# Kernel tuning notes

Measured on AMD Instinct MI355X. Metric: run time of the kernel, lower is better.

The kernel has to match this reference:

```python
import jax, jax.numpy as jnp
import numpy as np

B, T = 4096, 35          # batch rallies, max_ball_round
DSE = 227                # state_embed_dim = (37-2) + 64 + 64 + 64
C = 64                   # context_dim
H = 1024                 # hidden_dim
G5 = 25                  # GMM_num * 5
S = 12                   # shot_num
SE_NOCTX = DSE - C       # 163, state_embedding features before prior_z concat


def setup_inputs() -> dict:
    key = jax.random.key(0)
    ks = jax.random.split(key, 24)
    def r(i, shape, s=0.05):
        return (jax.random.normal(ks[i], shape, jnp.float32) * s)
    return {
        "state_embedding": r(0, (B, T, SE_NOCTX), 1.0),
        "prior_z": r(1, (B, C), 1.0),
        # state_ref_encoder (no bias)
        "W_ref": r(2, (T * DSE, DSE), 0.01),
        # f_decoder: DSE -> H -> H -> DSE with Softplus
        "fW1": r(3, (DSE, H)), "fb1": jnp.zeros((H,), jnp.float32),
        "fW2": r(4, (H, H)),   "fb2": jnp.zeros((H,), jnp.float32),
        "fW3": r(5, (H, DSE)), "fb3": jnp.zeros((DSE,), jnp.float32),
        # g_nets: DSE independent Linear(1,DSE)->Softplus->Linear(DSE,1)->Sigmoid, stacked
        "gW1": r(6, (DSE, DSE), 0.01), "gb1": r(7, (DSE, DSE), 0.01),
        "gW2": r(8, (DSE, DSE), 0.01), "gb2": r(9, (DSE,), 0.01),
        # GMM / shot heads on f_latent (no bias)
        "W_land": r(10, (DSE, G5), 0.01),
        "W_shot": r(11, (DSE, S), 0.01),
        "W_move": r(12, (DSE, G5), 0.01),
        # context_decoder: C -> H -> H -> C with Softplus
        "cW1": r(13, (C, H)), "cb1": jnp.zeros((H,), jnp.float32),
        "cW2": r(14, (H, H)), "cb2": jnp.zeros((H,), jnp.float32),
        "cW3": r(15, (H, C)), "cb3": jnp.zeros((C,), jnp.float32),
        # context GMM / shot heads (no bias)
        "cW_land": r(16, (C, G5), 0.01),
        "cW_shot": r(17, (C, S), 0.01),
        "cW_move": r(18, (C, G5), 0.01),
    }


def reference(state_embedding, prior_z, W_ref,
              fW1, fb1, fW2, fb2, fW3, fb3,
              gW1, gb1, gW2, gb2,
              W_land, W_shot, W_move,
              cW1, cb1, cW2, cb2, cW3, cb3,
              cW_land, cW_shot, cW_move):
    sp = jax.nn.softplus
    b, t, _ = state_embedding.shape

    # context_decoder(prior_z)
    ch = sp(prior_z @ cW1 + cb1)
    ch = sp(ch @ cW2 + cb2)
    ctx = ch @ cW3 + cb3                                  # [B, C]

    # repeat prior_z along time, concat, flatten, state_ref_encoder
    prior_rep = jnp.broadcast_to(prior_z[:, None, :], (b, t, prior_z.shape[-1]))
    sre = jnp.concatenate([state_embedding, prior_rep], axis=-1)  # [B, T, DSE]
    f_input = sre.reshape(b, -1) @ W_ref                  # [B, DSE]

    # f_decoder
    fh = sp(f_input @ fW1 + fb1)
    fh = sp(fh @ fW2 + fb2)
    f_latent = fh @ fW3 + fb3                             # [B, DSE]

    # g(): DSE per-dim tiny MLPs, fully vectorized as batched einsum
    gh = sp(f_latent[:, :, None] * gW1[None, :, :] + gb1[None, :, :])  # [B, DSE, DSE]
    g_out = jax.nn.sigmoid(jnp.einsum('bdh,dh->bd', gh, gW2) + gb2)    # [B, DSE]

    # GMM / shot heads
    land = f_latent @ W_land                              # [B, 25]
    shot = jax.nn.log_softmax(f_latent @ W_shot, axis=-1) # [B, 12]
    move = f_latent @ W_move                              # [B, 25]
    c_land = ctx @ cW_land
    c_shot = jax.nn.log_softmax(ctx @ cW_shot, axis=-1)
    c_move = ctx @ cW_move

    return jnp.concatenate([land, shot, move, g_out, c_land, c_shot, c_move, ctx], axis=-1)  # [B, 415]
```

## Files before the change

kernel.cpp:

```cpp
#include <hip/hip_runtime.h>
#include <hip/hip_bf16.h>

using s8 = __attribute__((ext_vector_type(8))) short;
using f4 = __attribute__((ext_vector_type(4))) float;
using us8 = __attribute__((ext_vector_type(8))) unsigned short;

__device__ __forceinline__ void glds16(const void* g, void* l) {
    __builtin_amdgcn_global_load_lds(
        (const __attribute__((address_space(1))) void*)g,
        (__attribute__((address_space(3))) void*)l, 16, 0, 0);
}

__device__ __forceinline__ unsigned short f2b(float f) {
    union { float f; unsigned u; } v; v.f = f;
    unsigned r = v.u + 0x7fffu + ((v.u >> 16) & 1u);
    return (unsigned short)(r >> 16);
}
__device__ __forceinline__ float softplus_f(float x) {
    return fmaxf(x, 0.f) + __logf(1.f + __expf(-fabsf(x)));
}
__device__ __forceinline__ float sigmoid_f(float x) {
    return 1.f / (1.f + __expf(-x));
}
__device__ __forceinline__ float exp2_f(float x) {
    float r; asm("v_exp_f32 %0, %1" : "=v"(r) : "v"(x)); return r;
}
__device__ __forceinline__ float log2_f(float x) {
    float r; asm("v_log_f32 %0, %1" : "=v"(r) : "v"(x)); return r;
}

__global__ __launch_bounds__(256) void transpose_w(const float* __restrict__ src,
                                                   unsigned short* __restrict__ dst,
                                                   int K, int N, int Kpad, int Npad) {
    __shared__ float tile[32][33];
    const int n0 = blockIdx.x * 32, k0 = blockIdx.y * 32;
    const int tx = threadIdx.x, ty = threadIdx.y;
#pragma unroll
    for (int r = 0; r < 4; r++) {
        int k = k0 + ty + r * 8, n = n0 + tx;
        tile[ty + r * 8][tx] = (k < K && n < N) ? src[(size_t)k * N + n] : 0.f;
    }
    __syncthreads();
#pragma unroll
    for (int r = 0; r < 4; r++) {
        int n = n0 + ty + r * 8, k = k0 + tx;
        if (n < Npad && k < Kpad) dst[(size_t)n * Kpad + k] = f2b(tile[tx][ty + r * 8]);
    }
}

__global__ __launch_bounds__(256) void prep6_k(
    const float* __restrict__ s0, const float* __restrict__ s1,
    const float* __restrict__ s2, const float* __restrict__ s3,
    const float* __restrict__ s4, const float* __restrict__ s5,
    unsigned short* __restrict__ d0, unsigned short* __restrict__ d1,
    unsigned short* __restrict__ d2, unsigned short* __restrict__ d3,
    unsigned short* __restrict__ d4, unsigned short* __restrict__ d5) {
    constexpr int Ks[6] = {64, 1024, 1024, 227, 1024, 1024};
    constexpr int Ns[6] = {1024, 1024, 64, 1024, 1024, 227};
    constexpr int Kp[6] = {64, 1024, 1024, 256, 1024, 1024};
    constexpr int Np[6] = {1024, 1024, 128, 1024, 1024, 256};
    const int z = blockIdx.z;
    const int K = Ks[z], N = Ns[z], Kpad = Kp[z], Npad = Np[z];
    if ((int)blockIdx.x >= Npad / 32 || (int)blockIdx.y >= Kpad / 32) return;
    const float* src = z == 0 ? s0 : z == 1 ? s1 : z == 2 ? s2 : z == 3 ? s3 : z == 4 ? s4 : s5;
    unsigned short* dst = z == 0 ? d0 : z == 1 ? d1 : z == 2 ? d2 : z == 3 ? d3 : z == 4 ? d4 : d5;
    __shared__ float tile[32][33];
    const int n0 = blockIdx.x * 32, k0 = blockIdx.y * 32;
    const int tx = threadIdx.x, ty = threadIdx.y;
#pragma unroll
    for (int r = 0; r < 4; r++) {
        int k = k0 + ty + r * 8, n = n0 + tx;
        tile[ty + r * 8][tx] = (k < K && n < N) ? src[(size_t)k * N + n] : 0.f;
    }
    __syncthreads();
#pragma unroll
    for (int r = 0; r < 4; r++) {
        int n = n0 + ty + r * 8, k = k0 + tx;
        dst[(size_t)n * Kpad + k] = f2b(tile[tx][ty + r * 8]);
    }
}

__global__ __launch_bounds__(256) void wcat_t(const float* __restrict__ Wref,
                                              unsigned short* __restrict__ dst) {
    __shared__ float tile[32][33];
    const int n0 = blockIdx.x * 32, k0 = blockIdx.y * 32;
    const int tx = threadIdx.x, ty = threadIdx.y;
#pragma unroll
    for (int r = 0; r < 4; r++) {
        int k = k0 + ty + r * 8, n = n0 + tx;
        float v = 0.f;
        if (n < 227 && k < 5769) {
            if (k < 5705) {
                int wrow = k + 64 * (k / 163);
                v = Wref[(size_t)wrow * 227 + n];
            } else {
                int j2 = k - 5705;
                for (int t = 0; t < 35; t++)
                    v += Wref[(size_t)(t * 227 + 163 + j2) * 227 + n];
            }
        }
        tile[ty + r * 8][tx] = v;
    }
    __syncthreads();
#pragma unroll
    for (int r = 0; r < 4; r++) {
        int n = n0 + ty + r * 8, k = k0 + tx;
        if (n < 256 && k < 5792) dst[(size_t)n * 5792 + k] = f2b(tile[tx][ty + r * 8]);
    }
}

__global__ __launch_bounds__(256) void misc_k(
    const float* __restrict__ pz, unsigned short* __restrict__ pzb,
    const float* __restrict__ gb1, const float* __restrict__ gW2,
    float* __restrict__ b1s, float* __restrict__ w2s,
    const float* __restrict__ Wl, const float* __restrict__ Ws, const float* __restrict__ Wm,
    const float* __restrict__ cWl, const float* __restrict__ cWs, const float* __restrict__ cWm,
    unsigned short* __restrict__ WhcT) {
    constexpr int NCVT = 4096 * 64;
    constexpr int NGS = 227 * 227;
    constexpr int NW = 128 * 320;
    int i = blockIdx.x * 256 + threadIdx.x;
    if (i < NCVT) {
        pzb[i] = f2b(pz[i]);
    } else if (i < NCVT + NGS) {
        int j = i - NCVT;
        b1s[j] = gb1[j] * 1.44269504f;
        w2s[j] = gW2[j] * 0.69314718f;
    } else if (i < NCVT + NGS + NW) {
        int j = i - NCVT - NGS;
        int n = j / 320, k = j - n * 320;
        float v = 0.f;
        if (n < 62 && k < 227) {
            if (n < 25)      v = Wl[(size_t)k * 25 + n];
            else if (n < 37) v = Ws[(size_t)k * 12 + (n - 25)];
            else             v = Wm[(size_t)k * 25 + (n - 37)];
        } else if (n >= 64 && n < 126 && k >= 256) {
            const int jj = n - 64, kk = k - 256;
            if (jj < 25)      v = cWl[(size_t)kk * 25 + jj];
            else if (jj < 37) v = cWs[(size_t)kk * 12 + (jj - 25)];
            else              v = cWm[(size_t)kk * 25 + (jj - 37)];
        }
        WhcT[(size_t)n * 320 + k] = f2b(v);
    }
}

__global__ __launch_bounds__(256) void acat_k8(const float* __restrict__ se,
                                               const float* __restrict__ pz,
                                               unsigned short* __restrict__ dst) {
    const int row = blockIdx.y;
    const int c = blockIdx.x * 256 + threadIdx.x;
    if (c >= 724) return;
    const int col0 = c * 8;
    us8 o;
    if (col0 + 8 <= 5705) {
        const float* s = se + (size_t)row * 5705 + col0;
#pragma unroll
        for (int j = 0; j < 8; j++) o[j] = f2b(s[j]);
    } else {
#pragma unroll
        for (int j = 0; j < 8; j++) {
            int col = col0 + j;
            float v = 0.f;
            if (col < 5705) v = se[(size_t)row * 5705 + col];
            else if (col < 5769) v = pz[(size_t)row * 64 + (col - 5705)];
            o[j] = f2b(v);
        }
    }
    *(us8*)(dst + (size_t)row * 5792 + col0) = o;
}

__global__ __launch_bounds__(256) void finb_k(const float* __restrict__ fin,
                                              unsigned short* __restrict__ out) {
    const int row = blockIdx.y, col = threadIdx.x;
    out[(size_t)row * 256 + col] = (col < 227) ? f2b(fin[(size_t)row * 228 + col])
                                               : (unsigned short)0;
}

__global__ __launch_bounds__(256) void fillb_k(float* __restrict__ buf,
                                               const float* __restrict__ bias,
                                               int ld, int ncr) {
    const int row = blockIdx.y;
    const int col = blockIdx.x * 256 + threadIdx.x;
    if (col >= ld) return;
    float v = 0.f;
    if (bias && col < ncr) v = bias[col];
    buf[(size_t)row * ld + col] = v;
}

__global__ __launch_bounds__(256) void gscale_k(const float* __restrict__ gb1,
                                                const float* __restrict__ gW2,
                                                float* __restrict__ b1s,
                                                float* __restrict__ w2s) {
    int i = blockIdx.x * 256 + threadIdx.x;
    if (i < 227 * 227) {
        b1s[i] = gb1[i] * 1.44269504f;
        w2s[i] = gW2[i] * 0.69314718f;
    }
}

__global__ __launch_bounds__(256) void red_enc4(const float* __restrict__ part,
                                                unsigned short* __restrict__ finb) {
    const int t = threadIdx.x;
    const int row = blockIdx.y * 4 + (t >> 6);
    const int cw = t & 63;
    if (cw < 57) {
        const float* p = part + (size_t)row * 228 + cw * 4;
        float4 s = make_float4(0.f, 0.f, 0.f, 0.f);
#pragma unroll
        for (int z = 0; z < 6; z++) {
            float4 v = *(const float4*)(p + (size_t)z * 4096 * 228);
            s.x += v.x; s.y += v.y; s.z += v.z; s.w += v.w;
        }
        if (cw == 56) s.w = 0.f;
        ushort4 o;
        o.x = f2b(s.x); o.y = f2b(s.y); o.z = f2b(s.z); o.w = f2b(s.w);
        *(ushort4*)(finb + (size_t)row * 256 + cw * 4) = o;
    } else {
        ushort4 z4 = make_ushort4(0, 0, 0, 0);
        *(ushort4*)(finb + (size_t)row * 256 + 228 + (cw - 57) * 4) = z4;
    }
}

__global__ __launch_bounds__(256) void red_cf3_k(
    const float* __restrict__ part_c3, const float* __restrict__ cb3,
    float* __restrict__ ctxb,
    const float* __restrict__ part_f3, const float* __restrict__ fb3,
    float* __restrict__ flat) {
    const int bx = blockIdx.x, t = threadIdx.x;
    if (bx < 256) {
        int idx = bx * 256 + t;
        int row = idx >> 4, c4 = idx & 15;
        float4 s = *(const float4*)(cb3 + c4 * 4);
        const float* p = part_c3 + (size_t)row * 64 + c4 * 4;
#pragma unroll
        for (int z = 0; z < 8; z++) {
            float4 v = *(const float4*)(p + (size_t)z * 4096 * 64);
            s.x += v.x; s.y += v.y; s.z += v.z; s.w += v.w;
        }
        *(float4*)(ctxb + (size_t)row * 64 + c4 * 4) = s;
    } else {
        const int by = bx - 256;
        const int row = by * 4 + (t >> 6);
        const int cw = t & 63;
        if (cw >= 57) return;
        float b[4];
#pragma unroll
        for (int j = 0; j < 4; j++) {
            int col = cw * 4 + j;
            b[j] = (col < 227) ? fb3[col] : 0.f;
        }
        const float* p = part_f3 + (size_t)row * 228 + cw * 4;
        float4 s = make_float4(b[0], b[1], b[2], b[3]);
#pragma unroll
        for (int z = 0; z < 4; z++) {
            float4 v = *(const float4*)(p + (size_t)z * 4096 * 228);
            s.x += v.x; s.y += v.y; s.z += v.z; s.w += v.w;
        }
        if (cw == 56) s.w = 0.f;
        *(float4*)(flat + (size_t)row * 228 + cw * 4) = s;
    }
}

__global__ __launch_bounds__(320) void ah_k(const float* __restrict__ flat,
                                            const float* __restrict__ ctx,
                                            unsigned short* __restrict__ dst) {
    const int b = blockIdx.x, t = threadIdx.x;
    float v = 0.f;
    if (t < 227) v = flat[(size_t)b * 228 + t];
    else if (t >= 256) v = ctx[(size_t)b * 64 + (t - 256)];
    dst[(size_t)b * 320 + t] = f2b(v);
}

__device__ __forceinline__ float lse12(const float* s) {
    float m = s[0];
#pragma unroll
    for (int j = 1; j < 12; j++) m = fmaxf(m, s[j]);
    float sum = 0.f;
#pragma unroll
    for (int j = 0; j < 12; j++) sum += __expf(s[j] - m);
    return m + __logf(sum);
}

__global__ __launch_bounds__(192) void final_k(const float* __restrict__ raw,
                                               const float* __restrict__ ctx,
                                               float* __restrict__ out) {
    __shared__ float s[12], c[12];
    const int b = blockIdx.x, t = threadIdx.x;
    float* ob = out + (size_t)b * 415;
    const float* rb = raw + (size_t)b * 128;
    if (t < 62) {
        float v = rb[t];
        if (t < 25) ob[t] = v;
        else if (t < 37) s[t - 25] = v;
        else ob[t] = v;
    } else if (t >= 64 && t < 126) {
        const int j2 = t - 64;
        float v = rb[t];
        if (j2 < 25) ob[289 + j2] = v;
        else if (j2 < 37) c[j2 - 25] = v;
        else ob[289 + j2] = v;
    } else if (t >= 128) {
        ob[351 + (t - 128)] = ctx[(size_t)b * 64 + (t - 128)];
    }
    __syncthreads();
    if (t < 12) {
        ob[25 + t] = s[t] - lse12(s);
    } else if (t >= 64 && t < 76) {
        ob[314 + (t - 64)] = c[t - 64] - lse12(c);
    }
}

template <int CM, int ACT, bool OBF16>
__global__ __launch_bounds__(256) void gemm_dma(
    const unsigned short* __restrict__ A, int lda,
    const unsigned short* __restrict__ WT, int ldwt,
    const float* __restrict__ bias,
    void* __restrict__ Cptr, int ldc, int N, int K, int kchunk) {
    __shared__ __align__(16) unsigned short As[128 * 32];
    __shared__ __align__(16) unsigned short Bs[128 * 32];
    const int tid = threadIdx.x;
    const int m0 = blockIdx.y * 128, n0 = blockIdx.x * 128;
    const int kbeg = blockIdx.z * kchunk;
    const int kend = min(kbeg + kchunk, K);
    const int lane = tid & 63, w = tid >> 6;
    const int wm = w >> 1, wn = w & 1;
    const int quad = lane >> 4, l16 = lane & 15;
    const int dr = lane >> 2;
    const int dk = (lane & 3) * 8;

    f4 acc[4][4] = {};

    for (int k0 = kbeg; k0 < kend; k0 += 32) {
#pragma unroll
        for (int c = 0; c < 2; c++) {
            int rr = w * 32 + c * 16;
            glds16(A + (size_t)(m0 + rr + dr) * lda + k0 + dk, &As[rr * 32]);
            glds16(WT + (size_t)(n0 + rr + dr) * ldwt + k0 + dk, &Bs[rr * 32]);
        }
        __syncthreads();
        s8 a[4], b[4];
#pragma unroll
        for (int mi = 0; mi < 4; mi++)
            a[mi] = *(const s8*)&As[(wm * 64 + mi * 16 + l16) * 32 + quad * 8];
#pragma unroll
        for (int ni = 0; ni < 4; ni++)
            b[ni] = *(const s8*)&Bs[(wn * 64 + ni * 16 + l16) * 32 + quad * 8];
#pragma unroll
        for (int mi = 0; mi < 4; mi++)
#pragma unroll
            for (int ni = 0; ni < 4; ni++)
                acc[mi][ni] = __builtin_amdgcn_mfma_f32_16x16x32_bf16(
                    a[mi], b[ni], acc[mi][ni], 0, 0, 0);
        __syncthreads();
    }

    const size_t zoff = (CM == 2) ? (size_t)blockIdx.z * 4096 * ldc : 0;
#pragma unroll
    for (int mi = 0; mi < 4; mi++) {
        int gmb = m0 + wm * 64 + mi * 16 + quad * 4;
#pragma unroll
        for (int ni = 0; ni < 4; ni++) {
            int gn = n0 + wn * 64 + ni * 16 + l16;
            if (gn < N) {
#pragma unroll
                for (int r = 0; r < 4; r++) {
                    float v = acc[mi][ni][r];
                    size_t off = (size_t)(gmb + r) * ldc + gn;
                    if (CM == 2) {
                        ((float*)Cptr)[zoff + off] = v;
                    } else {
                        if (bias) v += bias[gn];
                        if (ACT == 1) v = softplus_f(v);
                        if (OBF16) ((unsigned short*)Cptr)[off] = f2b(v);
                        else ((float*)Cptr)[off] = v;
                    }
                }
            }
        }
    }
}

__global__ __launch_bounds__(256) void gemm_dualg(
    const unsigned short* __restrict__ A0, int lda0, int K0,
    const unsigned short* __restrict__ A1, int lda1, int K1,
    const unsigned short* __restrict__ W0, int ldw0,
    const unsigned short* __restrict__ W1, int ldw1,
    const float* __restrict__ b0, const float* __restrict__ b1,
    unsigned short* __restrict__ C0, unsigned short* __restrict__ C1) {
    __shared__ __align__(16) unsigned short As[128 * 32];
    __shared__ __align__(16) unsigned short Bs[128 * 32];
    const int z = blockIdx.z;
// ... 37 lines not shown
                    a[mi], b[ni], acc[mi][ni], 0, 0, 0);
        __syncthreads();
    }

#pragma unroll
    for (int mi = 0; mi < 4; mi++) {
        int gmb = m0 + wm * 64 + mi * 16 + quad * 4;
#pragma unroll
        for (int ni = 0; ni < 4; ni++) {
            int gn = n0 + wn * 64 + ni * 16 + l16;
#pragma unroll
            for (int r = 0; r < 4; r++) {
                float v = acc[mi][ni][r] + bias[gn];
                C[(size_t)(gmb + r) * 1024 + gn] = f2b(softplus_f(v));
            }
        }
    }
}

__global__ __launch_bounds__(256) void part_cf3_k(
    const unsigned short* __restrict__ h2c, const unsigned short* __restrict__ cW3T,
    const unsigned short* __restrict__ h2f, const unsigned short* __restrict__ fW3T,
    float* __restrict__ part_c3, float* __restrict__ part_f3) {
    __shared__ __align__(16) unsigned short As[128 * 32];
    __shared__ __align__(16) unsigned short Bs[128 * 32];
    const int z = blockIdx.z;
    const bool isC = (z < 8);
    if (isC && blockIdx.x != 0) return;
    const unsigned short* __restrict__ A  = isC ? h2c : h2f;
    const unsigned short* __restrict__ WT = isC ? cW3T : fW3T;
    const int N   = isC ? 64 : 227;
    const int ldc = isC ? 64 : 228;
    const int zz  = isC ? z : z - 8;
    const int kbeg = zz * (isC ? 128 : 256);
    const int kend = kbeg + (isC ? 128 : 256);
    float* __restrict__ C = (isC ? part_c3 : part_f3) + (size_t)zz * 4096 * ldc;
    const int tid = threadIdx.x;
    const int m0 = blockIdx.y * 128, n0 = blockIdx.x * 128;
    const int lane = tid & 63, w = tid >> 6;
    const int wm = w >> 1, wn = w & 1;
    const int quad = lane >> 4, l16 = lane & 15;
    const int dr = lane >> 2;
    const int dk = (lane & 3) * 8;

    f4 acc[4][4] = {};

    for (int k0 = kbeg; k0 < kend; k0 += 32) {
#pragma unroll
        for (int c = 0; c < 2; c++) {
            int rr = w * 32 + c * 16;
            glds16(A + (size_t)(m0 + rr + dr) * 1024 + k0 + dk, &As[rr * 32]);
            glds16(WT + (size_t)(n0 + rr + dr) * 1024 + k0 + dk, &Bs[rr * 32]);
        }
        __syncthreads();
        s8 a[4], b[4];
#pragma unroll
        for (int mi = 0; mi < 4; mi++)
            a[mi] = *(const s8*)&As[(wm * 64 + mi * 16 + l16) * 32 + quad * 8];
#pragma unroll
        for (int ni = 0; ni < 4; ni++)
            b[ni] = *(const s8*)&Bs[(wn * 64 + ni * 16 + l16) * 32 + quad * 8];
#pragma unroll
        for (int mi = 0; mi < 4; mi++)
#pragma unroll
            for (int ni = 0; ni < 4; ni++)
                acc[mi][ni] = __builtin_amdgcn_mfma_f32_16x16x32_bf16(
                    a[mi], b[ni], acc[mi][ni], 0, 0, 0);
        __syncthreads();
    }

#pragma unroll
    for (int mi = 0; mi < 4; mi++) {
        int gmb = m0 + wm * 64 + mi * 16 + quad * 4;
#pragma unroll
        for (int ni = 0; ni < 4; ni++) {
            int gn = n0 + wn * 64 + ni * 16 + l16;
            if (gn < N) {
#pragma unroll
                for (int r = 0; r < 4; r++)
                    C[(size_t)(gmb + r) * ldc + gn] = acc[mi][ni][r];
            }
        }
    }
}

template <int AMODE, int ACT, bool ATOMIC, bool OBF16>
__global__ __launch_bounds__(256) void gemm_mfma(
    const void* __restrict__ Aptr, int lda,
    const float* __restrict__ A2ptr,
    const unsigned short* __restrict__ WT, int ldwt,
    const float* __restrict__ bias,
    void* __restrict__ Cptr, int ldc,
    int M, int N, int K, int kchunk) {
    __shared__ unsigned short As[128 * 40];
    __shared__ unsigned short Bs[128 * 40];
    const int tid = threadIdx.x;
    const int m0 = blockIdx.y * 128, n0 = blockIdx.x * 128;
    const int kbeg = blockIdx.z * kchunk;
    const int kend = min(kbeg + kchunk, K);
    const int lane = tid & 63, w = tid >> 6;
    const int wm = w >> 1, wn = w & 1;
    const int quad = lane >> 4, l16 = lane & 15;

    f4 acc[4][4] = {};
    ushort4 pa[4], pb[4];

    auto loadA = [&](int k0) {
        const bool full = (kend - k0) >= 32;
#pragma unroll
        for (int i = 0; i < 4; i++) {
            int f = tid + i * 256;
            int r = f >> 3, cc = (f & 7) * 4;
            int gm = m0 + r;
            ushort4 val;
            if (AMODE == 0) {
                const float* A = (const float*)Aptr;
                float t[4];
#pragma unroll
                for (int j = 0; j < 4; j++) {
                    int k = k0 + cc + j;
                    t[j] = (k < kend) ? A[(size_t)gm * lda + k] : 0.f;
                }
                val.x = f2b(t[0]); val.y = f2b(t[1]); val.z = f2b(t[2]); val.w = f2b(t[3]);
            } else if (AMODE == 1) {
                const unsigned short* A = (const unsigned short*)Aptr;
                if (full) {
                    val = *(const ushort4*)(A + (size_t)gm * lda + k0 + cc);
                } else {
                    unsigned short t[4];
#pragma unroll
                    for (int j = 0; j < 4; j++) {
                        int k = k0 + cc + j;
                        t[j] = (k < kend) ? A[(size_t)gm * lda + k] : (unsigned short)0;
                    }
                    val.x = t[0]; val.y = t[1]; val.z = t[2]; val.w = t[3];
                }
            } else {
                const float* se = (const float*)Aptr;
                float t[4];
#pragma unroll
                for (int j = 0; j < 4; j++) {
                    int k = k0 + cc + j;
                    float v = 0.f;
                    if (k < kend) {
                        v = (k < 5705) ? se[(size_t)gm * 5705 + k]
                                       : A2ptr[(size_t)gm * 64 + (k - 5705)];
                    }
                    t[j] = v;
                }
                val.x = f2b(t[0]); val.y = f2b(t[1]); val.z = f2b(t[2]); val.w = f2b(t[3]);
            }
            pa[i] = val;
        }
    };
    auto loadB = [&](int k0) {
        const bool full = (kend - k0) >= 32;
#pragma unroll
        for (int i = 0; i < 4; i++) {
            int f = tid + i * 256;
            int r = f >> 3, cc = (f & 7) * 4;
            int gn = n0 + r;
            ushort4 val;
            if (gn < N) {
                if (full) {
                    val = *(const ushort4*)(WT + (size_t)gn * ldwt + k0 + cc);
                } else {
// ... 139 lines not shown
            for (int k = 0; k < 64; k++) a = fmaf(cx[k], cWl[(size_t)k * 25 + j2], a);
            ob[289 + j2] = a;
        } else if (j2 < 37) {
            int j = j2 - 25;
            float a = 0.f;
            for (int k = 0; k < 64; k++) a = fmaf(cx[k], cWsh[(size_t)k * 12 + j], a);
            craw[j] = a;
        } else {
            int j = j2 - 37;
            float a = 0.f;
            for (int k = 0; k < 64; k++) a = fmaf(cx[k], cWm[(size_t)k * 25 + j], a);
            ob[326 + j] = a;
        }
    } else if (t >= 128 && t < 192) {
        ob[351 + (t - 128)] = cx[t - 128];
    }
    __syncthreads();
    if (t == 0) lsf = lse12(sraw);
    if (t == 64) lsc = lse12(craw);
    __syncthreads();
    if (t < 12) ob[25 + t] = sraw[t] - lsf;
    else if (t >= 64 && t < 76) ob[314 + (t - 64)] = craw[t - 64] - lsc;
}

extern "C" void kernel_launch(void* const* d_in, const int* in_sizes, int n_in,
                              void* d_out, int out_size, void* d_ws, size_t ws_size,
                              hipStream_t stream) {
    const float* se    = (const float*)d_in[0];
    const float* pz    = (const float*)d_in[1];
    const float* Wref  = (const float*)d_in[2];
    const float* fW1   = (const float*)d_in[3];
    const float* fb1   = (const float*)d_in[4];
    const float* fW2   = (const float*)d_in[5];
    const float* fb2   = (const float*)d_in[6];
    const float* fW3   = (const float*)d_in[7];
    const float* fb3   = (const float*)d_in[8];
    const float* gW1   = (const float*)d_in[9];
    const float* gb1   = (const float*)d_in[10];
    const float* gW2   = (const float*)d_in[11];
    const float* gb2   = (const float*)d_in[12];
    const float* Wland = (const float*)d_in[13];
    const float* Wshot = (const float*)d_in[14];
    const float* Wmove = (const float*)d_in[15];
    const float* cW1   = (const float*)d_in[16];
    const float* cb1   = (const float*)d_in[17];
    const float* cW2   = (const float*)d_in[18];
    const float* cb2   = (const float*)d_in[19];
    const float* cW3   = (const float*)d_in[20];
    const float* cb3   = (const float*)d_in[21];
    const float* cWl   = (const float*)d_in[22];
    const float* cWs   = (const float*)d_in[23];
    const float* cWm   = (const float*)d_in[24];
    float* out = (float*)d_out;
    const int M = 4096;

    char* p = (char*)d_ws;
    auto alloc = [&](size_t bytes) {
        char* r = p;
        p += (bytes + 255) & ~(size_t)255;
        return r;
    };
    unsigned short* WcatT = (unsigned short*)alloc((size_t)256 * 5792 * 2);
    unsigned short* cW1T  = (unsigned short*)alloc((size_t)1024 * 64 * 2);
    unsigned short* cW2T  = (unsigned short*)alloc((size_t)1024 * 1024 * 2);
    unsigned short* cW3T  = (unsigned short*)alloc((size_t)128 * 1024 * 2);
    unsigned short* fW1T  = (unsigned short*)alloc((size_t)1024 * 256 * 2);
    unsigned short* fW2T  = (unsigned short*)alloc((size_t)1024 * 1024 * 2);
    unsigned short* fW3T  = (unsigned short*)alloc((size_t)256 * 1024 * 2);
    float* fin  = (float*)alloc((size_t)M * 228 * 4);
    float* flat = (float*)alloc((size_t)M * 228 * 4);
    float* ctxb = (float*)alloc((size_t)M * 64 * 4);
    unsigned short* h2b  = (unsigned short*)alloc((size_t)M * 1024 * 2);
    unsigned short* h1fb = (unsigned short*)alloc((size_t)M * 1024 * 2);
    float* b1s = (float*)alloc((size_t)227 * 227 * 4);
    float* w2s = (float*)alloc((size_t)227 * 227 * 4);

    size_t base_used = (size_t)(p - (char*)d_ws);
    size_t full_extra = (size_t)M * 64 * 2
                      + (size_t)M * 256 * 2
                      + (size_t)M * 5792 * 2
                      + (size_t)128 * 320 * 2 + 1024;
    const bool full = (base_used + full_extra + 65536) <= ws_size;

    prep6_k<<<dim3(32, 32, 6), dim3(32, 8), 0, stream>>>(
        cW1, cW2, cW3, fW1, fW2, fW3, cW1T, cW2T, cW3T, fW1T, fW2T, fW3T);
    wcat_t<<<dim3(8, 181), dim3(32, 8), 0, stream>>>(Wref, WcatT);

    if (full) {
        unsigned short* pzb  = (unsigned short*)alloc((size_t)M * 64 * 2);
        unsigned short* finb = (unsigned short*)alloc((size_t)M * 256 * 2);
        char* region = alloc((size_t)M * 5792 * 2);
        unsigned short* WhcT = (unsigned short*)alloc((size_t)128 * 320 * 2);
        unsigned short* Acat = (unsigned short*)region;
        float* part_enc = fin;
        unsigned short* h2fb   = (unsigned short*)region;
        float* part_c3         = (float*)(region + (size_t)8 * 1024 * 1024);
        unsigned short* h1f    = (unsigned short*)(region + (size_t)16 * 1024 * 1024);
        float* part_f3         = (float*)(region + (size_t)24 * 1024 * 1024);
        float* rawfc           = (float*)(region + (size_t)39 * 1024 * 1024);
        unsigned short* Ah     = (unsigned short*)(region + (size_t)41 * 1024 * 1024);
        unsigned short* h1c = h1fb;
        unsigned short* h2c = h2b;

        misc_k<<<dim3(1386), 256, 0, stream>>>(
            pz, pzb, gb1, gW2, b1s, w2s, Wland, Wshot, Wmove, cWl, cWs, cWm, WhcT);
        acat_k8<<<dim3(3, M), 256, 0, stream>>>(se, pz, Acat);

        gemm_dma<2, 0, false><<<dim3(2, 32, 6), 256, 0, stream>>>(
            Acat, 5792, WcatT, 5792, nullptr, part_enc, 228, 227, 5792, 992);
        red_enc4<<<dim3(1, 1024), 256, 0, stream>>>(part_enc, finb);

        gemm_dualg<<<dim3(8, 32, 2), 256, 0, stream>>>(
            pzb, 64, 64, finb, 256, 256, cW1T, 64, fW1T, 256, cb1, fb1, h1c, h1f);
        gemm_dualg<<<dim3(8, 32, 2), 256, 0, stream>>>(
            h1c, 1024, 1024, h1f, 1024, 1024, cW2T, 1024, fW2T, 1024, cb2, fb2, h2c, h2fb);

        part_cf3_k<<<dim3(2, 32, 12), 256, 0, stream>>>(
            h2c, cW3T, h2fb, fW3T, part_c3, part_f3);
        red_cf3_k<<<dim3(1280), 256, 0, stream>>>(
            part_c3, cb3, ctxb, part_f3, fb3, flat);

        g_kernel2<<<dim3(227, 8), 256, 0, stream>>>(flat, gW1, b1s, w2s, gb2, out);

        ah_k<<<dim3(4096), 320, 0, stream>>>(flat, ctxb, Ah);
        gemm_dma<0, 0, false><<<dim3(1, 32, 1), 256, 0, stream>>>(
            Ah, 320, WhcT, 320, nullptr, rawfc, 128, 126, 320, 320);
        final_k<<<dim3(4096), 192, 0, stream>>>(rawfc, ctxb, out);
    } else {
        gscale_k<<<dim3(202), 256, 0, stream>>>(gb1, gW2, b1s, w2s);
        fillb_k<<<dim3(1, M), 256, 0, stream>>>(fin, nullptr, 228, 0);
        fillb_k<<<dim3(1, M), 256, 0, stream>>>(flat, fb3, 228, 227);
        fillb_k<<<dim3(1, M), 256, 0, stream>>>(ctxb, cb3, 64, 64);
        unsigned short* h1 = h1fb;
        gemm_mfma<0, 1, false, true><<<dim3(8, 32, 1), 256, 0, stream>>>(
            pz, 64, nullptr, cW1T, 64, cb1, h1, 1024, M, 1024, 64, 64);
        gemm_mfma<1, 1, false, true><<<dim3(8, 32, 1), 256, 0, stream>>>(
            h1, 1024, nullptr, cW2T, 1024, cb2, h2b, 1024, M, 1024, 1024, 1024);
        gemm_mfma<1, 0, true, false><<<dim3(1, 32, 8), 256, 0, stream>>>(
            h2b, 1024, nullptr, cW3T, 1024, nullptr, ctxb, 64, M, 64, 1024, 128);
        gemm_mfma<2, 0, true, false><<<dim3(2, 32, 8), 256, 0, stream>>>(
            se, 5705, pz, WcatT, 5792, nullptr, fin, 228, M, 227, 5769, 736);
        gemm_mfma<0, 1, false, true><<<dim3(8, 32, 1), 256, 0, stream>>>(
            fin, 228, nullptr, fW1T, 256, fb1, h1, 1024, M, 1024, 227, 227);
        gemm_mfma<1, 1, false, true><<<dim3(8, 32, 1), 256, 0, stream>>>(
            h1, 1024, nullptr, fW2T, 1024, fb2, h2b, 1024, M, 1024, 1024, 1024);
        gemm_mfma<1, 0, true, false><<<dim3(2, 32, 8), 256, 0, stream>>>(
            h2b, 1024, nullptr, fW3T, 1024, nullptr, flat, 228, M, 227, 1024, 128);
        heads_k<<<dim3(4096), 256, 0, stream>>>(flat, ctxb, Wland, Wshot, Wmove,
                                                cWl, cWs, cWm, out);
        g_kernel2<<<dim3(227, 8), 256, 0, stream>>>(flat, gW1, b1s, w2s, gb2, out);
    }
}
```

Before: 410.0 us.

## Merge prep kernels into one launch and fuse tail stages into fewer kernels

Combines the weight transposes, Wref concat-transpose, misc conversions and activation bf16 packing into a single prep_all_k launch partitioned by block index. It also fuses the g-net evaluation with building the head input, and fuses the heads GEMM with the log-softmax and output scatter, removing the rawfc round trip and the final_k launch. The aim is to cut launch overhead and intermediate global traffic, at the cost of more branching inside the merged kernels and blocks of uneven cost sharing one grid.

```diff
diff --git a/kernel.cpp b/kernel.cpp
--- a/kernel.cpp
+++ b/kernel.cpp
@@ -29,172 +29,142 @@
     float r; asm("v_log_f32 %0, %1" : "=v"(r) : "v"(x)); return r;
 }
 
-__global__ __launch_bounds__(256) void transpose_w(const float* __restrict__ src,
-                                                   unsigned short* __restrict__ dst,
-                                                   int K, int N, int Kpad, int Npad) {
-    __shared__ float tile[32][33];
-    const int n0 = blockIdx.x * 32, k0 = blockIdx.y * 32;
-    const int tx = threadIdx.x, ty = threadIdx.y;
-#pragma unroll
-    for (int r = 0; r < 4; r++) {
-        int k = k0 + ty + r * 8, n = n0 + tx;
-        tile[ty + r * 8][tx] = (k < K && n < N) ? src[(size_t)k * N + n] : 0.f;
-    }
-    __syncthreads();
-#pragma unroll
-    for (int r = 0; r < 4; r++) {
-        int n = n0 + ty + r * 8, k = k0 + tx;
-        if (n < Npad && k < Kpad) dst[(size_t)n * Kpad + k] = f2b(tile[tx][ty + r * 8]);
-    }
-}
-
-__global__ __launch_bounds__(256) void prep6_k(
-    const float* __restrict__ s0, const float* __restrict__ s1,
-    const float* __restrict__ s2, const float* __restrict__ s3,
-    const float* __restrict__ s4, const float* __restrict__ s5,
-    unsigned short* __restrict__ d0, unsigned short* __restrict__ d1,
-    unsigned short* __restrict__ d2, unsigned short* __restrict__ d3,
-    unsigned short* __restrict__ d4, unsigned short* __restrict__ d5) {
-    constexpr int Ks[6] = {64, 1024, 1024, 227, 1024, 1024};
-    constexpr int Ns[6] = {1024, 1024, 64, 1024, 1024, 227};
-    constexpr int Kp[6] = {64, 1024, 1024, 256, 1024, 1024};
-    constexpr int Np[6] = {1024, 1024, 128, 1024, 1024, 256};
-    const int z = blockIdx.z;
-    const int K = Ks[z], N = Ns[z], Kpad = Kp[z], Npad = Np[z];
-    if ((int)blockIdx.x >= Npad / 32 || (int)blockIdx.y >= Kpad / 32) return;
-    const float* src = z == 0 ? s0 : z == 1 ? s1 : z == 2 ? s2 : z == 3 ? s3 : z == 4 ? s4 : s5;
-    unsigned short* dst = z == 0 ? d0 : z == 1 ? d1 : z == 2 ? d2 : z == 3 ? d3 : z == 4 ? d4 : d5;
-    __shared__ float tile[32][33];
-    const int n0 = blockIdx.x * 32, k0 = blockIdx.y * 32;
-    const int tx = threadIdx.x, ty = threadIdx.y;
-#pragma unroll
-    for (int r = 0; r < 4; r++) {
-        int k = k0 + ty + r * 8, n = n0 + tx;
-        tile[ty + r * 8][tx] = (k < K && n < N) ? src[(size_t)k * N + n] : 0.f;
-    }
-    __syncthreads();
-#pragma unroll
-    for (int r = 0; r < 4; r++) {
-        int n = n0 + ty + r * 8, k = k0 + tx;
-        dst[(size_t)n * Kpad + k] = f2b(tile[tx][ty + r * 8]);
-    }
-}
-
-__global__ __launch_bounds__(256) void wcat_t(const float* __restrict__ Wref,
-                                              unsigned short* __restrict__ dst) {
-    __shared__ float tile[32][33];
-    const int n0 = blockIdx.x * 32, k0 = blockIdx.y * 32;
-    const int tx = threadIdx.x, ty = threadIdx.y;
-#pragma unroll
-    for (int r = 0; r < 4; r++) {
-        int k = k0 + ty + r * 8, n = n0 + tx;
-        float v = 0.f;
-        if (n < 227 && k < 5769) {
-            if (k < 5705) {
-                int wrow = k + 64 * (k / 163);
-                v = Wref[(size_t)wrow * 227 + n];
-            } else {
-                int j2 = k - 5705;
-                for (int t = 0; t < 35; t++)
-                    v += Wref[(size_t)(t * 227 + 163 + j2) * 227 + n];
-            }
-        }
-        tile[ty + r * 8][tx] = v;
-    }
-    __syncthreads();
-#pragma unroll
-    for (int r = 0; r < 4; r++) {
-        int n = n0 + ty + r * 8, k = k0 + tx;
-        if (n < 256 && k < 5792) dst[(size_t)n * 5792 + k] = f2b(tile[tx][ty + r * 8]);
-    }
-}
-
-__global__ __launch_bounds__(256) void misc_k(
+__device__ __forceinline__ float lse12(const float* s) {
+    float m = s[0];
+#pragma unroll
+    for (int j = 1; j < 12; j++) m = fmaxf(m, s[j]);
+    float sum = 0.f;
+#pragma unroll
+    for (int j = 0; j < 12; j++) sum += __expf(s[j] - m);
+    return m + __logf(sum);
+}
+
+__global__ __launch_bounds__(256) void prep_all_k(
+    const float* __restrict__ cW1, const float* __restrict__ cW2,
+    const float* __restrict__ cW3, const float* __restrict__ fW1,
+    const float* __restrict__ fW2, const float* __restrict__ fW3,
+    unsigned short* __restrict__ cW1T, unsigned short* __restrict__ cW2T,
+    unsigned short* __restrict__ cW3T, unsigned short* __restrict__ fW1T,
+    unsigned short* __restrict__ fW2T, unsigned short* __restrict__ fW3T,
+    const float* __restrict__ Wref, unsigned short* __restrict__ WcatT,
     const float* __restrict__ pz, unsigned short* __restrict__ pzb,
     const float* __restrict__ gb1, const float* __restrict__ gW2,
     float* __restrict__ b1s, float* __restrict__ w2s,
-    const float* __restrict__ Wl, const float* __restrict__ Ws, const float* __restrict__ Wm,
-    const float* __restrict__ cWl, const float* __restrict__ cWs, const float* __restrict__ cWm,
-    unsigned short* __restrict__ WhcT) {
-    constexpr int NCVT = 4096 * 64;
-    constexpr int NGS = 227 * 227;
-    constexpr int NW = 128 * 320;
-    int i = blockIdx.x * 256 + threadIdx.x;
-    if (i < NCVT) {
-        pzb[i] = f2b(pz[i]);
-    } else if (i < NCVT + NGS) {
-        int j = i - NCVT;
-        b1s[j] = gb1[j] * 1.44269504f;
-        w2s[j] = gW2[j] * 0.69314718f;
-    } else if (i < NCVT + NGS + NW) {
-        int j = i - NCVT - NGS;
-        int n = j / 320, k = j - n * 320;
-        float v = 0.f;
-        if (n < 62 && k < 227) {
-            if (n < 25)      v = Wl[(size_t)k * 25 + n];
-            else if (n < 37) v = Ws[(size_t)k * 12 + (n - 25)];
-            else             v = Wm[(size_t)k * 25 + (n - 37)];
-        } else if (n >= 64 && n < 126 && k >= 256) {
-            const int jj = n - 64, kk = k - 256;
-            if (jj < 25)      v = cWl[(size_t)kk * 25 + jj];
-            else if (jj < 37) v = cWs[(size_t)kk * 12 + (jj - 25)];
-            else              v = cWm[(size_t)kk * 25 + (jj - 37)];
-        }
-        WhcT[(size_t)n * 320 + k] = f2b(v);
-    }
-}
-
-__global__ __launch_bounds__(256) void acat_k8(const float* __restrict__ se,
-                                               const float* __restrict__ pz,
-                                               unsigned short* __restrict__ dst) {
-    const int row = blockIdx.y;
-    const int c = blockIdx.x * 256 + threadIdx.x;
-    if (c >= 724) return;
-    const int col0 = c * 8;
-    us8 o;
-    if (col0 + 8 <= 5705) {
-        const float* s = se + (size_t)row * 5705 + col0;
-#pragma unroll
-        for (int j = 0; j < 8; j++) o[j] = f2b(s[j]);
+    const float* __restrict__ Wl, const float* __restrict__ Ws,
+    const float* __restrict__ Wm, const float* __restrict__ cWl,
+    const float* __restrict__ cWs, const float* __restrict__ cWm,
+    unsigned short* __restrict__ WhcT,
+    const float* __restrict__ se, unsigned short* __restrict__ Acat) {
+    __shared__ float tile[32][33];
+    const int b = blockIdx.x, t = threadIdx.x;
+    if (b < 2752) {
+        int z, r = b;
+        if (r < 64) { z = 0; }
+        else if (r < 1088) { z = 1; r -= 64; }
+        else if (r < 1216) { z = 2; r -= 1088; }
+        else if (r < 1472) { z = 3; r -= 1216; }
+        else if (r < 2496) { z = 4; r -= 1472; }
+        else { z = 5; r -= 2496; }
+        const float* src = z == 0 ? cW1 : z == 1 ? cW2 : z == 2 ? cW3
+                          : z == 3 ? fW1 : z == 4 ? fW2 : fW3;
+        unsigned short* dst = z == 0 ? cW1T : z == 1 ? cW2T : z == 2 ? cW3T
+                             : z == 3 ? fW1T : z == 4 ? fW2T : fW3T;
+        const int K    = z == 0 ? 64 : z == 3 ? 227 : 1024;
+        const int N    = z == 2 ? 64 : z == 5 ? 227 : 1024;
+        const int Kpad = z == 0 ? 64 : z == 3 ? 256 : 1024;
+        const int Npad = z == 2 ? 128 : z == 5 ? 256 : 1024;
+        const int nbx = Npad >> 5;
+        const int bx = r % nbx, by = r / nbx;
+        const int n0 = bx * 32, k0 = by * 32;
+        const int tx = t & 31, ty = t >> 5;
+#pragma unroll
+        for (int rr = 0; rr < 4; rr++) {
+            int k = k0 + ty + rr * 8, n = n0 + tx;
+            tile[ty + rr * 8][tx] = (k < K && n < N) ? src[(size_t)k * N + n] : 0.f;
+        }
+        __syncthreads();
+#pragma unroll
+        for (int rr = 0; rr < 4; rr++) {
+            int n = n0 + ty + rr * 8, k = k0 + tx;
+            dst[(size_t)n * Kpad + k] = f2b(tile[tx][ty + rr * 8]);
+        }
+    } else if (b < 4200) {
+        const int r = b - 2752;
+        const int n0 = (r & 7) * 32, k0 = (r >> 3) * 32;
+        const int tx = t & 31, ty = t >> 5;
+#pragma unroll
+        for (int rr = 0; rr < 4; rr++) {
+            int k = k0 + ty + rr * 8, n = n0 + tx;
+            float v = 0.f;
+            if (n < 227 && k < 5769) {
+                if (k < 5705) {
+                    int wrow = k + 64 * (k / 163);
+                    v = Wref[(size_t)wrow * 227 + n];
+                } else {
+                    int j2 = k - 5705;
+                    for (int tt = 0; tt < 35; tt++)
+                        v += Wref[(size_t)(tt * 227 + 163 + j2) * 227 + n];
+                }
+            }
+            tile[ty + rr * 8][tx] = v;
+        }
+        __syncthreads();
+#pragma unroll
+        for (int rr = 0; rr < 4; rr++) {
+            int n = n0 + ty + rr * 8, k = k0 + tx;
+            if (n < 256 && k < 5792) dst_write: ;
+            if (n < 256 && k < 5792)
+                WcatT[(size_t)n * 5792 + k] = f2b(tile[tx][ty + rr * 8]);
+        }
+    } else if (b < 5586) {
+        constexpr int NCVT = 4096 * 64;
+        constexpr int NGS = 227 * 227;
+        constexpr int NW = 128 * 320;
+        int i = (b - 4200) * 256 + t;
+        if (i < NCVT) {
+            pzb[i] = f2b(pz[i]);
+        } else if (i < NCVT + NGS) {
+            int j = i - NCVT;
+            b1s[j] = gb1[j] * 1.44269504f;
+            w2s[j] = gW2[j] * 0.69314718f;
+        } else if (i < NCVT + NGS + NW) {
+            int j = i - NCVT - NGS;
+            int n = j / 320, k = j - n * 320;
+            float v = 0.f;
+            if (n < 62 && k < 227) {
+                if (n < 25)      v = Wl[(size_t)k * 25 + n];
+                else if (n < 37) v = Ws[(size_t)k * 12 + (n - 25)];
+                else             v = Wm[(size_t)k * 25 + (n - 37)];
+            } else if (n >= 64 && n < 126 && k >= 256) {
+                const int jj = n - 64, kk = k - 256;
+                if (jj < 25)      v = cWl[(size_t)kk * 25 + jj];
+                else if (jj < 37) v = cWs[(size_t)kk * 12 + (jj - 25)];
+                else              v = cWm[(size_t)kk * 25 + (jj - 37)];
+            }
+            WhcT[(size_t)n * 320 + k] = f2b(v);
+        }
     } else {
-#pragma unroll
-        for (int j = 0; j < 8; j++) {
-            int col = col0 + j;
-            float v = 0.f;
-            if (col < 5705) v = se[(size_t)row * 5705 + col];
-            else if (col < 5769) v = pz[(size_t)row * 64 + (col - 5705)];
-            o[j] = f2b(v);
-        }
-    }
-    *(us8*)(dst + (size_t)row * 5792 + col0) = o;
-}
-
-__global__ __launch_bounds__(256) void finb_k(const float* __restrict__ fin,
-                                              unsigned short* __restrict__ out) {
-    const int row = blockIdx.y, col = threadIdx.x;
-    out[(size_t)row * 256 + col] = (col < 227) ? f2b(fin[(size_t)row * 228 + col])
-                                               : (unsigned short)0;
-}
-
-__global__ __launch_bounds__(256) void fillb_k(float* __restrict__ buf,
-                                               const float* __restrict__ bias,
-                                               int ld, int ncr) {
-    const int row = blockIdx.y;
-    const int col = blockIdx.x * 256 + threadIdx.x;
-    if (col >= ld) return;
-    float v = 0.f;
-    if (bias && col < ncr) v = bias[col];
-    buf[(size_t)row * ld + col] = v;
-}
-
-__global__ __launch_bounds__(256) void gscale_k(const float* __restrict__ gb1,
-                                                const float* __restrict__ gW2,
-                                                float* __restrict__ b1s,
-                                                float* __restrict__ w2s) {
-    int i = blockIdx.x * 256 + threadIdx.x;
-    if (i < 227 * 227) {
-        b1s[i] = gb1[i] * 1.44269504f;
-        w2s[i] = gW2[i] * 0.69314718f;
+        const int r = b - 5586;
+        const int c = (r % 3) * 256 + t;
+        const int row = r / 3;
+        if (c >= 724) return;
+        const int col0 = c * 8;
+        us8 o;
+        if (col0 + 8 <= 5705) {
+            const float* s = se + (size_t)row * 5705 + col0;
+#pragma unroll
+            for (int j = 0; j < 8; j++) o[j] = f2b(s[j]);
+        } else {
+#pragma unroll
+            for (int j = 0; j < 8; j++) {
+                int col = col0 + j;
+                float v = 0.f;
+                if (col < 5705) v = se[(size_t)row * 5705 + col];
+                else if (col < 5769) v = pz[(size_t)row * 64 + (col - 5705)];
+                o[j] = f2b(v);
+            }
+        }
+        *(us8*)(Acat + (size_t)row * 5792 + col0) = o;
     }
 }
 
@@ -258,55 +228,6 @@
         }
         if (cw == 56) s.w = 0.f;
         *(float4*)(flat + (size_t)row * 228 + cw * 4) = s;
-    }
-}
-
-__global__ __launch_bounds__(320) void ah_k(const float* __restrict__ flat,
-                                            const float* __restrict__ ctx,
-                                            unsigned short* __restrict__ dst) {
-    const int b = blockIdx.x, t = threadIdx.x;
-    float v = 0.f;
-    if (t < 227) v = flat[(size_t)b * 228 + t];
-    else if (t >= 256) v = ctx[(size_t)b * 64 + (t - 256)];
-    dst[(size_t)b * 320 + t] = f2b(v);
-}
-
-__device__ __forceinline__ float lse12(const float* s) {
-    float m = s[0];
-#pragma unroll
-    for (int j = 1; j < 12; j++) m = fmaxf(m, s[j]);
-    float sum = 0.f;
-#pragma unroll
-    for (int j = 0; j < 12; j++) sum += __expf(s[j] - m);
-    return m + __logf(sum);
-}
-
-__global__ __launch_bounds__(192) void final_k(const float* __restrict__ raw,
-                                               const float* __restrict__ ctx,
-                                               float* __restrict__ out) {
-    __shared__ float s[12], c[12];
-    const int b = blockIdx.x, t = threadIdx.x;
-    float* ob = out + (size_t)b * 415;
-    const float* rb = raw + (size_t)b * 128;
-    if (t < 62) {
-        float v = rb[t];
-        if (t < 25) ob[t] = v;
-        else if (t < 37) s[t - 25] = v;
-        else ob[t] = v;
-    } else if (t >= 64 && t < 126) {
-        const int j2 = t - 64;
-        float v = rb[t];
-        if (j2 < 25) ob[289 + j2] = v;
-        else if (j2 < 37) c[j2 - 25] = v;
-        else ob[289 + j2] = v;
-    } else if (t >= 128) {
-        ob[351 + (t - 128)] = ctx[(size_t)b * 64 + (t - 128)];
-    }
-    __syncthreads();
-    if (t < 12) {
-        ob[25 + t] = s[t] - lse12(s);
-    } else if (t >= 64 && t < 76) {
-        ob[314 + (t - 64)] = c[t - 64] - lse12(c);
     }
 }
 
@@ -510,6 +431,206 @@
             }
         }
     }
+}
+
+__global__ __launch_bounds__(256) void tail_k(
+    const float* __restrict__ flat,
+    const float* __restrict__ gW1, const float* __restrict__ b1s,
+    const float* __restrict__ w2s, const float* __restrict__ gb2,
+    const float* __restrict__ ctxb, unsigned short* __restrict__ Ah,
+    float* __restrict__ out) {
+    __shared__ float4 wt[228];
+    const int bid = blockIdx.x, t = threadIdx.x;
+    if (bid < 1816) {
+        const int d = bid >> 3;
+        const int y = bid & 7;
+        if (t < 227) {
+            size_t o = (size_t)d * 227 + t;
+            wt[t] = make_float4(gW1[o], b1s[o], w2s[o], 0.f);
+        } else if (t == 227) {
+            wt[227] = make_float4(0.f, 0.f, 0.f, 0.f);
+        }
+        __syncthreads();
+        const int b0 = y * 512 + t;
+        float x0 = flat[(size_t)b0 * 228 + d] * 1.44269504f;
+        float x1 = flat[(size_t)(b0 + 256) * 228 + d] * 1.44269504f;
+        const float g2 = gb2[d];
+        float a0 = g2, a1 = g2;
+        float4 w = wt[0];
+#pragma unroll 2
+        for (int h = 0; h < 227; h++) {
+            float4 wn = wt[h + 1];
+            float z0 = fmaf(x0, w.x, w.y);
+            float z1 = fmaf(x1, w.x, w.y);
+            a0 = fmaf(log2_f(1.f + exp2_f(z0)), w.z, a0);
+            a1 = fmaf(log2_f(1.f + exp2_f(z1)), w.z, a1);
+            w = wn;
+        }
+        out[(size_t)b0 * 415 + 62 + d] = sigmoid_f(a0);
+        out[(size_t)(b0 + 256) * 415 + 62 + d] = sigmoid_f(a1);
+    } else {
+        const int row = bid - 1816;
+        float v = 0.f;
+        if (t < 227) v = flat[(size_t)row * 228 + t];
+        Ah[(size_t)row * 320 + t] = f2b(v);
+        if (t < 64) Ah[(size_t)row * 320 + 256 + t] = f2b(ctxb[(size_t)row * 64 + t]);
+    }
+}
+
+__global__ __launch_bounds__(256) void gemm_heads_k(
+    const unsigned short* __restrict__ Ah, const unsigned short* __restrict__ WhcT,
+    const float* __restrict__ ctxb, float* __restrict__ out) {
+    __shared__ __align__(16) unsigned short As[128 * 32];
+    __shared__ __align__(16) unsigned short Bs[128 * 32];
+    __shared__ float cT[64][129];
+    const int tid = threadIdx.x;
+    const int m0 = blockIdx.x * 128;
+    const int lane = tid & 63, w = tid >> 6;
+    const int wm = w >> 1, wn = w & 1;
+    const int quad = lane >> 4, l16 = lane & 15;
+    const int dr = lane >> 2;
+    const int dk = (lane & 3) * 8;
+
+    f4 acc[4][4] = {};
+
+    for (int k0 = 0; k0 < 320; k0 += 32) {
+#pragma unroll
+        for (int c = 0; c < 2; c++) {
+            int rr = w * 32 + c * 16;
+            glds16(Ah + (size_t)(m0 + rr + dr) * 320 + k0 + dk, &As[rr * 32]);
+            glds16(WhcT + (size_t)(rr + dr) * 320 + k0 + dk, &Bs[rr * 32]);
+        }
+        __syncthreads();
+        s8 a[4], b[4];
+#pragma unroll
+        for (int mi = 0; mi < 4; mi++)
+            a[mi] = *(const s8*)&As[(wm * 64 + mi * 16 + l16) * 32 + quad * 8];
+#pragma unroll
+        for (int ni = 0; ni < 4; ni++)
+            b[ni] = *(const s8*)&Bs[(wn * 64 + ni * 16 + l16) * 32 + quad * 8];
+#pragma unroll
+        for (int mi = 0; mi < 4; mi++)
+#pragma unroll
+            for (int ni = 0; ni < 4; ni++)
+                acc[mi][ni] = __builtin_amdgcn_mfma_f32_16x16x32_bf16(
+                    a[mi], b[ni], acc[mi][ni], 0, 0, 0);
+        __syncthreads();
+    }
+
+#pragma unroll
+    for (int pass = 0; pass < 2; pass++) {
+        if (wm == pass) {
+#pragma unroll
+            for (int mi = 0; mi < 4; mi++) {
+                int rl = mi * 16 + quad * 4;
+#pragma unroll
+                for (int ni = 0; ni < 4; ni++) {
+                    int cl = wn * 64 + ni * 16 + l16;
+#pragma unroll
+                    for (int r = 0; r < 4; r++)
+                        cT[rl + r][cl] = acc[mi][ni][r];
+                }
+            }
+        }
+        __syncthreads();
+        if (tid < 64) {
+            const int bidx = m0 + pass * 64 + tid;
+            float* ob = out + (size_t)bidx * 415;
+            const float* row = cT[tid];
+            float sraw[12], craw[12];
+#pragma unroll
+            for (int j = 0; j < 25; j++) ob[j] = row[j];
+#pragma unroll
+            for (int j = 0; j < 12; j++) sraw[j] = row[25 + j];
+#pragma unroll
+            for (int j = 0; j < 25; j++) ob[37 + j] = row[37 + j];
+#pragma unroll
+            for (int j = 0; j < 25; j++) ob[289 + j] = row[64 + j];
+#pragma unroll
+            for (int j = 0; j < 12; j++) craw[j] = row[89 + j];
+#pragma unroll
+            for (int j = 0; j < 25; j++) ob[326 + j] = row[101 + j];
+            const float lsf = lse12(sraw), lsc = lse12(craw);
+#pragma unroll
+            for (int j = 0; j < 12; j++) {
+                ob[25 + j] = sraw[j] - lsf;
+                ob[314 + j] = craw[j] - lsc;
+            }
+            for (int k = 0; k < 64; k++)
+                ob[351 + k] = ctxb[(size_t)bidx * 64 + k];
+        }
+        __syncthreads();
+    }
+}
+
+__global__ __launch_bounds__(256) void transpose_w(const float* __restrict__ src,
+                                                   unsigned short* __restrict__ dst,
+                                                   int K, int N, int Kpad, int Npad) {
+    __shared__ float tile[32][33];
+    const int n0 = blockIdx.x * 32, k0 = blockIdx.y * 32;
+    const int tx = threadIdx.x, ty = threadIdx.y;
+#pragma unroll
+    for (int r = 0; r < 4; r++) {
+        int k = k0 + ty + r * 8, n = n0 + tx;
+        tile[ty + r * 8][tx] = (k < K && n < N) ? src[(size_t)k * N + n] : 0.f;
+    }
+    __syncthreads();
+#pragma unroll
+    for (int r = 0; r < 4; r++) {
+        int n = n0 + ty + r * 8, k = k0 + tx;
+        if (n < Npad && k < Kpad) dst[(size_t)n * Kpad + k] = f2b(tile[tx][ty + r * 8]);
+    }
+}
+
+__global__ __launch_bounds__(256) void wcat_t(const float* __restrict__ Wref,
+                                              unsigned short* __restrict__ dst) {
+    __shared__ float tile[32][33];
+    const int n0 = blockIdx.x * 32, k0 = blockIdx.y * 32;
+    const int tx = threadIdx.x, ty = threadIdx.y;
+#pragma unroll
+    for (int r = 0; r < 4; r++) {
+        int k = k0 + ty + r * 8, n = n0 + tx;
+        float v = 0.f;
+        if (n < 227 && k < 5769) {
+            if (k < 5705) {
+                int wrow = k + 64 * (k / 163);
+                v = Wref[(size_t)wrow * 227 + n];
+            } else {
+                int j2 = k - 5705;
+                for (int t = 0; t < 35; t++)
+                    v += Wref[(size_t)(t * 227 + 163 + j2) * 227 + n];
+            }
+        }
+        tile[ty + r * 8][tx] = v;
+    }
+    __syncthreads();
+#pragma unroll
+    for (int r = 0; r < 4; r++) {
+        int n = n0 + ty + r * 8, k = k0 + tx;
+        if (n < 256 && k < 5792) dst[(size_t)n * 5792 + k] = f2b(tile[tx][ty + r * 8]);
+    }
+}
+
+__global__ __launch_bounds__(256) void gscale_k(const float* __restrict__ gb1,
+                                                const float* __restrict__ gW2,
+                                                float* __restrict__ b1s,
+                                                float* __restrict__ w2s) {
+    int i = blockIdx.x * 256 + threadIdx.x;
+    if (i < 227 * 227) {
+        b1s[i] = gb1[i] * 1.44269504f;
+        w2s[i] = gW2[i] * 0.69314718f;
+    }
+}
+
+__global__ __launch_bounds__(256) void fillb_k(float* __restrict__ buf,
+                                               const float* __restrict__ bias,
+                                               int ld, int ncr) {
+    const int row = blockIdx.y;
+    const int col = blockIdx.x * 256 + threadIdx.x;
+    if (col >= ld) return;
+    float v = 0.f;
+    if (bias && col < ncr) v = bias[col];
+    buf[(size_t)row * ld + col] = v;
 }
 
 template <int AMODE, int ACT, bool ATOMIC, bool OBF16>
@@ -815,10 +936,6 @@
                       + (size_t)128 * 320 * 2 + 1024;
     const bool full = (base_used + full_extra + 65536) <= ws_size;
 
-    prep6_k<<<dim3(32, 32, 6), dim3(32, 8), 0, stream>>>(
-        cW1, cW2, cW3, fW1, fW2, fW3, cW1T, cW2T, cW3T, fW1T, fW2T, fW3T);
-    wcat_t<<<dim3(8, 181), dim3(32, 8), 0, stream>>>(Wref, WcatT);
-
     if (full) {
         unsigned short* pzb  = (unsigned short*)alloc((size_t)M * 64 * 2);
         unsigned short* finb = (unsigned short*)alloc((size_t)M * 256 * 2);
@@ -830,14 +947,14 @@
         float* part_c3         = (float*)(region + (size_t)8 * 1024 * 1024);
         unsigned short* h1f    = (unsigned short*)(region + (size_t)16 * 1024 * 1024);
         float* part_f3         = (float*)(region + (size_t)24 * 1024 * 1024);
-        float* rawfc           = (float*)(region + (size_t)39 * 1024 * 1024);
         unsigned short* Ah     = (unsigned short*)(region + (size_t)41 * 1024 * 1024);
         unsigned short* h1c = h1fb;
         unsigned short* h2c = h2b;
 
-        misc_k<<<dim3(1386), 256, 0, stream>>>(
-            pz, pzb, gb1, gW2, b1s, w2s, Wland, Wshot, Wmove, cWl, cWs, cWm, WhcT);
-        acat_k8<<<dim3(3, M), 256, 0, stream>>>(se, pz, Acat);
+        prep_all_k<<<dim3(17874), 256, 0, stream>>>(
+            cW1, cW2, cW3, fW1, fW2, fW3, cW1T, cW2T, cW3T, fW1T, fW2T, fW3T,
+            Wref, WcatT, pz, pzb, gb1, gW2, b1s, w2s,
+            Wland, Wshot, Wmove, cWl, cWs, cWm, WhcT, se, Acat);
 
         gemm_dma<2, 0, false><<<dim3(2, 32, 6), 256, 0, stream>>>(
             Acat, 5792, WcatT, 5792, nullptr, part_enc, 228, 227, 5792, 992);
@@ -853,13 +970,19 @@
         red_cf3_k<<<dim3(1280), 256, 0, stream>>>(
             part_c3, cb3, ctxb, part_f3, fb3, flat);
 
-        g_kernel2<<<dim3(227, 8), 256, 0, stream>>>(flat, gW1, b1s, w2s, gb2, out);
-
-        ah_k<<<dim3(4096), 320, 0, stream>>>(flat, ctxb, Ah);
-        gemm_dma<0, 0, false><<<dim3(1, 32, 1), 256, 0, stream>>>(
-            Ah, 320, WhcT, 320, nullptr, rawfc, 128, 126, 320, 320);
-        final_k<<<dim3(4096), 192, 0, stream>>>(rawfc, ctxb, out);
+        tail_k<<<dim3(5912), 256, 0, stream>>>(
+            flat, gW1, b1s, w2s, gb2, ctxb, Ah, out);
+
+        gemm_heads_k<<<dim3(32), 256, 0, stream>>>(Ah, WhcT, ctxb, out);
     } else {
+        const dim3 tb(32, 8);
+        transpose_w<<<dim3(32, 2),  tb, 0, stream>>>(cW1, cW1T, 64, 1024, 64, 1024);
+        transpose_w<<<dim3(32, 32), tb, 0, stream>>>(cW2, cW2T, 1024, 1024, 1024, 1024);
+        transpose_w<<<dim3(4, 32),  tb, 0, stream>>>(cW3, cW3T, 1024, 64, 1024, 128);
+        transpose_w<<<dim3(32, 8),  tb, 0, stream>>>(fW1, fW1T, 227, 1024, 256, 1024);
+        transpose_w<<<dim3(32, 32), tb, 0, stream>>>(fW2, fW2T, 1024, 1024, 1024, 1024);
+        transpose_w<<<dim3(8, 32),  tb, 0, stream>>>(fW3, fW3T, 1024, 227, 1024, 256);
+        wcat_t<<<dim3(8, 181), tb, 0, stream>>>(Wref, WcatT);
         gscale_k<<<dim3(202), 256, 0, stream>>>(gb1, gW2, b1s, w2s);
         fillb_k<<<dim3(1, M), 256, 0, stream>>>(fin, nullptr, 228, 0);
         fillb_k<<<dim3(1, M), 256, 0, stream>>>(flat, fb3, 228, 227);
```

Measured after the change: 379.1 us. 1.08x faster.
